# Optimization experiments

Measured on AMD Instinct MI355X. Metric: run time of the kernel, lower is better.

The kernel has to match this reference:

```python
import jax, jax.numpy as jnp
import numpy as np

D_MODEL = 1024
N_HEADS = 16
FEA = 512
BATCH = 16
D_FF = 2048
HALF = D_MODEL // 2  # d_model / 2**fd_num with fd_num=1
INV_SQRT2 = 1.0 / np.sqrt(2.0).astype(np.float32)


def conv1d_circ(x, w, b):
    # x: (B, C_in, L); w: (C_out, C_in, 3); circular padding of 1 each side
    xp = jnp.pad(x, ((0, 0), (0, 0), (1, 1)), mode='wrap')
    y = jax.lax.conv_general_dilated(xp, w, (1,), 'VALID',
                                     dimension_numbers=('NCH', 'OIH', 'NCH'))
    return y + b[None, :, None]


def layer_norm(x, g, b):
    m = jnp.mean(x, axis=-1, keepdims=True)
    v = jnp.mean((x - m) ** 2, axis=-1, keepdims=True)
    return (x - m) / jnp.sqrt(v + 1e-5) * g + b


def setup_inputs() -> dict:
    key = jax.random.key(0)
    ks = jax.random.split(key, 16)
    s = 0.02
    inp = {
        'x': jax.random.normal(ks[0], (BATCH, FEA, D_MODEL), dtype=jnp.float32),
        'Wq': jax.random.normal(ks[1], (D_MODEL, HALF, 3), dtype=jnp.float32) * s,
        'bq': jnp.zeros((D_MODEL,), jnp.float32),
        'Wk': jax.random.normal(ks[2], (D_MODEL, HALF, 3), dtype=jnp.float32) * s,
        'bk': jnp.zeros((D_MODEL,), jnp.float32),
        'Wv': jax.random.normal(ks[3], (D_MODEL, HALF, 3), dtype=jnp.float32) * s,
        'bv': jnp.zeros((D_MODEL,), jnp.float32),
        'uns_w': jax.random.normal(ks[4], (FEA, 2 * FEA, 3), dtype=jnp.float32) * s,
        'uns_b': jnp.zeros((FEA,), jnp.float32),
        'cv_w1': jax.random.normal(ks[5], (D_FF, D_MODEL, 3), dtype=jnp.float32) * s,
        'cv_b1': jnp.zeros((D_FF,), jnp.float32),
        'cv_w2': jax.random.normal(ks[6], (HALF, D_FF, 3), dtype=jnp.float32) * s,
        'cv_b2': jnp.zeros((HALF,), jnp.float32),
        'cv_g': jnp.ones((HALF,), jnp.float32),
        'cv_beta': jnp.zeros((HALF,), jnp.float32),
        'up_w1': jax.random.normal(ks[7], (D_FF, HALF, 3), dtype=jnp.float32) * s,
        'up_b1': jnp.zeros((D_FF,), jnp.float32),
        'up_w2': jax.random.normal(ks[8], (D_MODEL, D_FF, 3), dtype=jnp.float32) * s,
        'up_b2': jnp.zeros((D_MODEL,), jnp.float32),
        'up_g': jnp.ones((D_MODEL,), jnp.float32),
        'up_beta': jnp.zeros((D_MODEL,), jnp.float32),
    }
    return inp


def reference(x, Wq, bq, Wk, bk, Wv, bv, uns_w, uns_b,
              cv_w1, cv_b1, cv_w2, cv_b2, cv_g, cv_beta,
              up_w1, up_b1, up_w2, up_b2, up_g, up_beta):
    x_input = x
    # torch code detaches x before the wavelet transform -> no grad through this branch
    xd = jax.lax.stop_gradient(x)
    # Haar (db1) single-level DWT along last axis (even length -> exact pairwise)
    x1 = (xd[..., 0::2] + xd[..., 1::2]) * INV_SQRT2  # cA: (B, F, HALF)
    x2 = (xd[..., 0::2] - xd[..., 1::2]) * INV_SQRT2  # cD: (B, F, HALF)

    def proj(z, w, b):  # (B, F, HALF) -> (B, F, D_MODEL)
        return conv1d_circ(z.swapaxes(1, 2), w, b).swapaxes(1, 2)

    def heads(z):  # (B, F, D_MODEL) -> (B, H, F, dh)
        b_, f_, _ = z.shape
        return z.reshape(b_, f_, N_HEADS, -1).transpose(0, 2, 1, 3)

    qh, kh, vh = heads(proj(x1, Wq, bq)), heads(proj(x1, Wk, bk)), heads(proj(x1, Wv, bv))
    ql, kl, vl = heads(proj(x2, Wq, bq)), heads(proj(x2, Wk, bk)), heads(proj(x2, Wv, bv))

    scale = 1.0 / np.sqrt(N_HEADS).astype(np.float32)  # note: module scales by sqrt(n_heads)
    b_, f_ = x.shape[0], x.shape[1]

    hp = jax.nn.softmax(jnp.einsum('bhqd,bhkd->bhqk', qh, kl) * scale, axis=-1)
    h_ctx = jnp.einsum('bhqk,bhkd->bhqd', hp, vh).transpose(0, 2, 1, 3).reshape(b_, f_, -1)
    lp = jax.nn.softmax(jnp.einsum('bhqd,bhkd->bhqk', ql, kh) * scale, axis=-1)
    l_ctx = jnp.einsum('bhqk,bhkd->bhqd', lp, vl).transpose(0, 2, 1, 3).reshape(b_, f_, -1)

    ctx = jnp.concatenate([h_ctx, l_ctx], axis=1)          # (B, 2F, D_MODEL)
    ctx = conv1d_circ(ctx, uns_w, uns_b)                    # channels=2F -> F, length=D_MODEL

    # Convlayer: conv over fea axis, channels D_MODEL -> D_FF -> HALF, then LN
    h = conv1d_circ(ctx.swapaxes(1, 2), cv_w1, cv_b1)
    h = conv1d_circ(jax.nn.relu(h), cv_w2, cv_b2)
    ctx = layer_norm(h.swapaxes(1, 2), cv_g, cv_beta)       # (B, F, HALF)

    # upsizeConvlayer: HALF -> D_FF -> D_MODEL, then LN
    h = conv1d_circ(ctx.swapaxes(1, 2), up_w1, up_b1)
    h = conv1d_circ(jax.nn.relu(h), up_w2, up_b2)
    out = layer_norm(h.swapaxes(1, 2), up_g, up_beta)       # (B, F, D_MODEL)
    return out + x_input
```

## Files before the change

kernel.cpp:

```cpp
#include <hip/hip_runtime.h>
#include <hip/hip_bf16.h>

#define B_    16
#define FEA_  512
#define DM_   1024
#define HALF_ 512
#define DFF_  2048

typedef unsigned short u16;
typedef __attribute__((ext_vector_type(8))) short bf16x8;
typedef __attribute__((ext_vector_type(4))) float f32x4;

__device__ __forceinline__ float bf2f(u16 u) {
  union { unsigned int i; float f; } v; v.i = ((unsigned int)u) << 16; return v.f;
}
__device__ __forceinline__ u16 f2bf(float f) {
  union { float f; unsigned int i; } v; v.f = f;
  unsigned int x = v.i;
  return (u16)((x + 0x7fffu + ((x >> 16) & 1u)) >> 16);
}
__device__ __forceinline__ void gload16(const u16* g, u16* l) {
  __builtin_amdgcn_global_load_lds(
      (const __attribute__((address_space(1))) void*)g,
      (__attribute__((address_space(3))) void*)l, 16, 0, 0);
}

__global__ void dwt_kernel(const float* __restrict__ x, u16* __restrict__ x1,
                           u16* __restrict__ x2, int n) {
  int i = blockIdx.x * 256 + threadIdx.x;
  if (i >= n) return;
  float2 v = ((const float2*)x)[i];
  x1[i] = f2bf((v.x + v.y) * 0.70710678118f);
  x2[i] = f2bf((v.x - v.y) * 0.70710678118f);
}

__global__ void wtrans3_kernel(const float* __restrict__ w0, const float* __restrict__ w1,
                               const float* __restrict__ w2, u16* __restrict__ wt,
                               int Cout, int Cin) {
  int n = Cout * Cin * 3;
  int e = blockIdx.x * 256 + threadIdx.x;
  if (e >= 3 * n) return;
  int i = e / n, le = e - i * n;
  const float* w = (i == 0) ? w0 : ((i == 1) ? w1 : w2);
  int co = le / (Cin * 3);
  int r  = le - co * Cin * 3;
  int ci = r / 3;
  int t  = r - ci * 3;
  wt[(size_t)i * n + ((size_t)t * Cout + co) * Cin + ci] = f2bf(w[le]);
}

struct WTSeg { const float* src; u16* dst; int cout, cin, base; };
struct WT5 { WTSeg s[5]; int total; };
__global__ void wtrans5_kernel(WT5 p) {
  int e = blockIdx.x * 256 + threadIdx.x;
  if (e >= p.total) return;
#pragma unroll
  for (int i = 0; i < 5; ++i) {
    int Cin = p.s[i].cin, Cout = p.s[i].cout;
    int n = Cout * Cin * 3;
    int le = e - p.s[i].base;
    if (le >= 0 && le < n) {
      int co = le / (Cin * 3);
      int r  = le - co * Cin * 3;
      int ci = r / 3;
      int t  = r - ci * 3;
      p.s[i].dst[((size_t)t * Cout + co) * Cin + ci] = f2bf(p.s[i].src[le]);
    }
  }
}

#define ZS_GLOAD(c0_)                                                        \
  {                                                                          \
    _Pragma("unroll") for (int i_ = 0; i_ < 5; ++i_) {                       \
      int e_ = tid + i_ * 256;                                               \
      if (e_ < 130 * 8) {                                                    \
        int r_ = e_ >> 3, c_ = e_ & 7;                                       \
        int gl_ = l0 + r_ - 1;                                               \
        if (gl_ < 0) gl_ += L; else if (gl_ >= L) gl_ -= L;                  \
        gload16(Zb + (size_t)gl_ * Cin + (c0_) + ((c_ ^ (r_ & 7)) * 8),      \
                smem + ((size_t)(i_ * 256 + (tid & 192)) * 8));              \
      }                                                                      \
    }                                                                        \
  }
#define WS_ISSUE(t_, c0_, buf_)                                              \
  {                                                                          \
    const u16* Wg_ = Wt + ((size_t)(t_) * Cout + co0) * Cin + (c0_);         \
    int c_ = lane & 7;                                                       \
    _Pragma("unroll") for (int i_ = 0; i_ < 4; ++i_) {                       \
      int rw_ = (i_ * 4 + w) * 8 + (lane >> 3);                              \
      gload16(Wg_ + (size_t)rw_ * Cin + ((c_ ^ (rw_ & 7)) * 8),              \
              &Wb[(buf_)][(i_ * 4 + w) * 8][0]);                             \
    }                                                                        \
  }
#define COMPUTE(t_, buf_)                                                    \
  {                                                                          \
    _Pragma("unroll") for (int ks = 0; ks < 2; ++ks) {                       \
      int s = ks * 4 + g4;                                                   \
      bf16x8 af[4], bfr[4];                                                  \
      _Pragma("unroll") for (int mi = 0; mi < 4; ++mi) {                     \
        int ra = wr * 64 + mi * 16 + row16 + (t_);                           \
        af[mi] = *(const bf16x8*)&Zs[ra][(s ^ (ra & 7)) * 8];                \
      }                                                                      \
      _Pragma("unroll") for (int ni = 0; ni < 4; ++ni) {                     \
        int rb = wc * 64 + ni * 16 + row16;                                  \
        bfr[ni] = *(const bf16x8*)&Wb[(buf_)][rb][(s ^ (rb & 7)) * 8];       \
      }                                                                      \
      __builtin_amdgcn_s_setprio(1);                                         \
      _Pragma("unroll") for (int mi = 0; mi < 4; ++mi)                       \
        _Pragma("unroll") for (int ni = 0; ni < 4; ++ni)                     \
          acc[mi][ni] = __builtin_amdgcn_mfma_f32_16x16x32_bf16(             \
              af[mi], bfr[ni], acc[mi][ni], 0, 0, 0);                        \
      __builtin_amdgcn_s_setprio(0);                                         \
    }                                                                        \
  }
#define COMPUTE2_REG(buf_)                                                   \
  {                                                                          \
    _Pragma("unroll") for (int ks = 0; ks < 2; ++ks) {                       \
      int s = ks * 4 + g4;                                                   \
      bf16x8 bfr[4];                                                         \
      _Pragma("unroll") for (int ni = 0; ni < 4; ++ni) {                     \
        int rb = wc * 64 + ni * 16 + row16;                                  \
        bfr[ni] = *(const bf16x8*)&Wb[(buf_)][rb][(s ^ (rb & 7)) * 8];       \
      }                                                                      \
      __builtin_amdgcn_s_setprio(1);                                         \
      _Pragma("unroll") for (int mi = 0; mi < 4; ++mi)                       \
        _Pragma("unroll") for (int ni = 0; ni < 4; ++ni)                     \
          acc[mi][ni] = __builtin_amdgcn_mfma_f32_16x16x32_bf16(             \
              af2[ks * 4 + mi], bfr[ni], acc[mi][ni], 0, 0, 0);              \
      __builtin_amdgcn_s_setprio(0);                                         \
    }                                                                        \
  }
#define WAIT4 { asm volatile("s_waitcnt vmcnt(4)" ::: "memory");             \
                __builtin_amdgcn_s_barrier(); }

__global__ __launch_bounds__(256, 2) void conv_mfma_kernel(
    const u16* __restrict__ Z, const u16* __restrict__ Wt,
    const float* __restrict__ bias, u16* __restrict__ out,
    int L, int Cin, int Cout, int osl, int osc, int relu) {
  __shared__ __align__(16) u16 smem[130 * 64 + 3 * 128 * 64];
  u16 (*Zs)[64] = (u16(*)[64])smem;
  u16 (*Wb)[128][64] = (u16(*)[128][64])(smem + 130 * 64);
  int l0 = blockIdx.x * 128, co0 = blockIdx.y * 128, b = blockIdx.z;
  int tid = threadIdx.x;
  int lane = tid & 63, w = tid >> 6, wr = w >> 1, wc = w & 1;
  int row16 = lane & 15, g4 = lane >> 4;
  f32x4 acc[4][4];
#pragma unroll
  for (int i = 0; i < 4; ++i)
#pragma unroll
    for (int j = 0; j < 4; ++j) acc[i][j] = (f32x4){0.f, 0.f, 0.f, 0.f};
  const u16* Zb = Z + (size_t)b * L * Cin;

  int ncg = Cin >> 6;
  ZS_GLOAD(0);
  WS_ISSUE(0, 0, 0);
  WS_ISSUE(1, 0, 1);

  for (int cg = 0; cg < ncg; ++cg) {
    int c0 = cg << 6;
    bool lastg = (cg == ncg - 1);
    WAIT4;
    WS_ISSUE(2, c0, 2);
    COMPUTE(0, 0);
    WAIT4;
    if (!lastg) WS_ISSUE(0, c0 + 64, 0);
    COMPUTE(1, 1);
    if (!lastg) {
      WAIT4;
      bf16x8 af2[8];
#pragma unroll
      for (int ks = 0; ks < 2; ++ks) {
        int s = ks * 4 + g4;
#pragma unroll
        for (int mi = 0; mi < 4; ++mi) {
          int ra = wr * 64 + mi * 16 + row16 + 2;
          af2[ks * 4 + mi] = *(const bf16x8*)&Zs[ra][(s ^ (ra & 7)) * 8];
        }
      }
      __builtin_amdgcn_sched_barrier(0);
      asm volatile("s_waitcnt lgkmcnt(0)" ::: "memory");
      __builtin_amdgcn_s_barrier();
      ZS_GLOAD(c0 + 64);
      WS_ISSUE(1, c0 + 64, 1);
      COMPUTE2_REG(2);
    } else {
      asm volatile("s_waitcnt vmcnt(0)" ::: "memory");
      __builtin_amdgcn_s_barrier();
      COMPUTE(2, 2);
    }
  }

  __syncthreads();
  const int TP = 136;
  u16* tile = smem;
  size_t ob = (size_t)b * L * Cout;
  int S, rowbase, colbase;
  if (osc == 1) { S = osl; rowbase = l0; colbase = co0; }
  else          { S = osc; rowbase = co0; colbase = l0; }
#pragma unroll
  for (int ni = 0; ni < 4; ++ni) {
    int c_loc = wc * 64 + ni * 16 + row16;
    float bz = bias[co0 + c_loc];
#pragma unroll
    for (int mi = 0; mi < 4; ++mi) {
#pragma unroll
      for (int r = 0; r < 4; ++r) {
        int l_loc = wr * 64 + mi * 16 + g4 * 4 + r;
        float v = acc[mi][ni][r] + bz;
        if (relu) v = fmaxf(v, 0.f);
        int row = (osc == 1) ? l_loc : c_loc;
        int col = (osc == 1) ? c_loc : l_loc;
        tile[row * TP + col] = f2bf(v);
      }
    }
  }
  __syncthreads();
  for (int e = tid; e < 128 * 16; e += 256) {
    int row = e >> 4, c8 = (e & 15) * 8;
    *(uint4*)(out + ob + (size_t)(rowbase + row) * S + colbase + c8) =
        *(const uint4*)&tile[row * TP + c8];
  }
}

__global__ __launch_bounds__(256, 4) void attn_mfma_kernel(
    const u16* __restrict__ qh, const u16* __restrict__ kh, const u16* __restrict__ vhT,
    const u16* __restrict__ ql, const u16* __restrict__ kl, const u16* __restrict__ vlT,
    u16* __restrict__ ctx) {
  __shared__ u16 Qs[64][72], Ks[64][72], Vts[64][72];
  __shared__ u16 Ps[64][72];
  __shared__ float rsl[2][2][32];
  int qt = blockIdx.x, h = blockIdx.y, bz = blockIdx.z;
  int b = bz >> 1, br = bz & 1;
  const u16* Q  = br ? ql  : qh;
  const u16* K  = br ? kh  : kl;
  const u16* Vt = br ? vlT : vhT;
  int tid = threadIdx.x;
  int lane = tid & 63, w = tid >> 6, wr = w >> 1, wc = w & 1;
  int row16 = lane & 15, g4 = lane >> 4, k8 = g4 * 8;
  int q0 = qt * 64;
  size_t baseQK = (size_t)b * FEA_ * DM_ + h * 64;
  size_t baseV  = (size_t)b * DM_ * FEA_ + (size_t)(h * 64) * FEA_;
  for (int e = tid; e < 64 * 8; e += 256) {
    int r = e >> 3, c = e & 7;
    *(uint4*)&Qs[r][c * 8] = *(const uint4*)(Q + baseQK + (size_t)(q0 + r) * DM_ + c * 8);
  }
  f32x4 oacc[2][2];
  float rsum[2][4];
#pragma unroll
  for (int i = 0; i < 2; ++i) {
#pragma unroll
    for (int j = 0; j < 2; ++j) oacc[i][j] = (f32x4){0.f, 0.f, 0.f, 0.f};
#pragma unroll
    for (int r = 0; r < 4; ++r) rsum[i][r] = 0.f;
  }
  for (int kt = 0; kt < 8; ++kt) {
    __syncthreads();
    for (int e = tid; e < 64 * 8; e += 256) {
      int r = e >> 3, c = e & 7;
      *(uint4*)&Ks[r][c * 8]  = *(const uint4*)(K + baseQK + (size_t)(kt * 64 + r) * DM_ + c * 8);
      *(uint4*)&Vts[r][c * 8] = *(const uint4*)(Vt + baseV + (size_t)r * FEA_ + kt * 64 + c * 8);
    }
    __syncthreads();
    f32x4 sacc[2][2];
#pragma unroll
    for (int i = 0; i < 2; ++i)
#pragma unroll
      for (int j = 0; j < 2; ++j) sacc[i][j] = (f32x4){0.f, 0.f, 0.f, 0.f};
#pragma unroll
    for (int ks = 0; ks < 2; ++ks) {
      int k0 = ks * 32 + k8;
      bf16x8 a0 = *(const bf16x8*)&Qs[wr * 32 + row16][k0];
      bf16x8 a1 = *(const bf16x8*)&Qs[wr * 32 + 16 + row16][k0];
      bf16x8 b0 = *(const bf16x8*)&Ks[wc * 32 + row16][k0];
      bf16x8 b1 = *(const bf16x8*)&Ks[wc * 32 + 16 + row16][k0];
      sacc[0][0] = __builtin_amdgcn_mfma_f32_16x16x32_bf16(a0, b0, sacc[0][0], 0, 0, 0);
      sacc[0][1] = __builtin_amdgcn_mfma_f32_16x16x32_bf16(a0, b1, sacc[0][1], 0, 0, 0);
      sacc[1][0] = __builtin_amdgcn_mfma_f32_16x16x32_bf16(a1, b0, sacc[1][0], 0, 0, 0);
      sacc[1][1] = __builtin_amdgcn_mfma_f32_16x16x32_bf16(a1, b1, sacc[1][1], 0, 0, 0);
    }
#pragma unroll
    for (int mi = 0; mi < 2; ++mi)
#pragma unroll
      for (int ni = 0; ni < 2; ++ni)
#pragma unroll
        for (int r = 0; r < 4; ++r) {
          float p = __expf(sacc[mi][ni][r] * 0.25f);
          rsum[mi][r] += p;
          Ps[wr * 32 + mi * 16 + g4 * 4 + r][wc * 32 + ni * 16 + row16] = f2bf(p);
        }
    __syncthreads();
#pragma unroll
    for (int ks = 0; ks < 2; ++ks) {
      int k0 = ks * 32 + k8;
      bf16x8 a0 = *(const bf16x8*)&Ps[wr * 32 + row16][k0];
      bf16x8 a1 = *(const bf16x8*)&Ps[wr * 32 + 16 + row16][k0];
      bf16x8 b0 = *(const bf16x8*)&Vts[wc * 32 + row16][k0];
      bf16x8 b1 = *(const bf16x8*)&Vts[wc * 32 + 16 + row16][k0];
      oacc[0][0] = __builtin_amdgcn_mfma_f32_16x16x32_bf16(a0, b0, oacc[0][0], 0, 0, 0);
      oacc[0][1] = __builtin_amdgcn_mfma_f32_16x16x32_bf16(a0, b1, oacc[0][1], 0, 0, 0);
      oacc[1][0] = __builtin_amdgcn_mfma_f32_16x16x32_bf16(a1, b0, oacc[1][0], 0, 0, 0);
      oacc[1][1] = __builtin_amdgcn_mfma_f32_16x16x32_bf16(a1, b1, oacc[1][1], 0, 0, 0);
    }
  }
#pragma unroll
  for (int mi = 0; mi < 2; ++mi)
#pragma unroll
    for (int r = 0; r < 4; ++r) {
#pragma unroll
      for (int m = 1; m < 16; m <<= 1) rsum[mi][r] += __shfl_xor(rsum[mi][r], m);
    }
  if (row16 == 0) {
#pragma unroll
    for (int mi = 0; mi < 2; ++mi)
#pragma unroll
      for (int r = 0; r < 4; ++r) rsl[wr][wc][mi * 16 + g4 * 4 + r] = rsum[mi][r];
  }
  __syncthreads();
#pragma unroll
  for (int mi = 0; mi < 2; ++mi)
#pragma unroll
    for (int ni = 0; ni < 2; ++ni)
#pragma unroll
      for (int r = 0; r < 4; ++r) {
        int qq = mi * 16 + g4 * 4 + r;
        float denom = rsl[wr][0][qq] + rsl[wr][1][qq];
        float o = oacc[mi][ni][r] / denom;
        Ps[wc * 32 + ni * 16 + row16][wr * 32 + qq] = f2bf(o);
      }
  __syncthreads();
  for (int e = tid; e < 64 * 8; e += 256) {
    int r = e >> 3, c = e & 7;
    size_t dst = ((size_t)b * DM_ + h * 64 + r) * (2 * FEA_) + br * 512 + q0 + c * 8;
    *(uint4*)(ctx + dst) = *(const uint4*)&Ps[r][c * 8];
  }
}

template <int RESID>
__global__ void ln_kernel(const u16* __restrict__ in, const float* __restrict__ g,
                          const float* __restrict__ beta, const float* __restrict__ resid,
                          void* __restrict__ outp, int C) {
  int row = blockIdx.x;
  int tid = threadIdx.x;
  const u16* p = in + (size_t)row * C;
  float s = 0.f, ss = 0.f;
  for (int c = tid * 4; c < C; c += 1024) {
    ushort4 u = *(const ushort4*)(p + c);
    float v0 = bf2f(u.x), v1 = bf2f(u.y), v2 = bf2f(u.z), v3 = bf2f(u.w);
    s += v0 + v1 + v2 + v3;
    ss += v0 * v0 + v1 * v1 + v2 * v2 + v3 * v3;
  }
#pragma unroll
  for (int m = 1; m < 64; m <<= 1) { s += __shfl_xor(s, m); ss += __shfl_xor(ss, m); }
  __shared__ float red[2][4];
  int wid = tid >> 6, lane = tid & 63;
  if (lane == 0) { red[0][wid] = s; red[1][wid] = ss; }
  __syncthreads();
  s  = red[0][0] + red[0][1] + red[0][2] + red[0][3];
  ss = red[1][0] + red[1][1] + red[1][2] + red[1][3];
  float m  = s / C;
  float var = ss / C - m * m;
  float inv = rsqrtf(var + 1e-5f);
  for (int c = tid * 4; c < C; c += 1024) {
    ushort4 u = *(const ushort4*)(p + c);
    float4 gg = *(const float4*)(g + c);
    float4 bb = *(const float4*)(beta + c);
    float v0 = (bf2f(u.x) - m) * inv * gg.x + bb.x;
    float v1 = (bf2f(u.y) - m) * inv * gg.y + bb.y;
    float v2 = (bf2f(u.z) - m) * inv * gg.z + bb.z;
    float v3 = (bf2f(u.w) - m) * inv * gg.w + bb.w;
    if (RESID) {
      float4 rr = *(const float4*)(resid + (size_t)row * C + c);
      float4 o = {v0 + rr.x, v1 + rr.y, v2 + rr.z, v3 + rr.w};
      *(float4*)((float*)outp + (size_t)row * C + c) = o;
    } else {
      ushort4 o = {f2bf(v0), f2bf(v1), f2bf(v2), f2bf(v3)};
      *(ushort4*)((u16*)outp + (size_t)row * C + c) = o;
    }
  }
}

extern "C" void kernel_launch(void* const* d_in, const int* in_sizes, int n_in,
                              void* d_out, int out_size, void* d_ws, size_t ws_size,
                              hipStream_t stream) {
  (void)in_sizes; (void)n_in; (void)out_size; (void)ws_size;
  const float* x      = (const float*)d_in[0];
  const float* Wq     = (const float*)d_in[1];
  const float* bq     = (const float*)d_in[2];
  const float* Wk     = (const float*)d_in[3];
  const float* bk     = (const float*)d_in[4];
  const float* Wv     = (const float*)d_in[5];
  const float* bv     = (const float*)d_in[6];
  const float* uns_w  = (const float*)d_in[7];
  const float* uns_b  = (const float*)d_in[8];
  const float* cv_w1  = (const float*)d_in[9];
  const float* cv_b1  = (const float*)d_in[10];
  const float* cv_w2  = (const float*)d_in[11];
  const float* cv_b2  = (const float*)d_in[12];
  const float* cv_g   = (const float*)d_in[13];
  const float* cv_beta= (const float*)d_in[14];
  const float* up_w1  = (const float*)d_in[15];
  const float* up_b1  = (const float*)d_in[16];
  const float* up_w2  = (const float*)d_in[17];
  const float* up_b2  = (const float*)d_in[18];
  const float* up_g   = (const float*)d_in[19];
  const float* up_beta= (const float*)d_in[20];

  char* ws = (char*)d_ws;
  const size_t MB = 1ull << 20;
  u16* x1    = (u16*)(ws + 0);
  u16* x1x2  = x1;
  u16* qhb   = (u16*)(ws + 16 * MB);
  u16* khb   = (u16*)(ws + 48 * MB);
  u16* vhb   = (u16*)(ws + 80 * MB);
  u16* qlb   = (u16*)(ws + 32 * MB);
  u16* klb   = (u16*)(ws + 64 * MB);
  u16* vlb   = (u16*)(ws + 96 * MB);
  u16* wt_proj = (u16*)d_out;
  u16* ctx   = (u16*)d_out;
  u16* wt_uns  = (u16*)(ws + 0);
  u16* wt_cv1  = (u16*)(ws + 4 * MB);
  u16* wt_cv2  = (u16*)(ws + 17 * MB);
  u16* wt_up1  = (u16*)(ws + 24 * MB);
  u16* wt_up2  = (u16*)(ws + 31 * MB);
  u16* ctx2  = (u16*)(ws + 48 * MB);
  u16* h1    = (u16*)(ws + 64 * MB);
  u16* h2    = (u16*)(ws + 96 * MB);
  u16* ctx3  = (u16*)(ws + 104 * MB);
  u16* h3    = (u16*)(ws + 64 * MB);
  u16* h4    = (u16*)(ws + 48 * MB);

  dwt_kernel<<<(B_ * FEA_ * HALF_ + 255) / 256, 256, 0, stream>>>(x, x1, (u16*)(ws + 8 * MB),
                                                                  B_ * FEA_ * HALF_);

  const int NPROJ = DM_ * HALF_ * 3;
  wtrans3_kernel<<<(3 * NPROJ + 255) / 256, 256, 0, stream>>>(Wq, Wk, Wv, wt_proj, DM_, HALF_);

  auto conv = [&](const u16* Z, const u16* wt, const float* bias, u16* out, int L,
                  int Cin, int Cout, int osl, int osc, int relu, int nb) {
    conv_mfma_kernel<<<dim3(L / 128, Cout / 128, nb), 256, 0, stream>>>(
        Z, wt, bias, out, L, Cin, Cout, osl, osc, relu);
  };

  conv(x1x2, wt_proj,              bq, qhb, FEA_, HALF_, DM_, DM_, 1, 0, 32);
  conv(x1x2, wt_proj + NPROJ,      bk, khb, FEA_, HALF_, DM_, DM_, 1, 0, 32);
  conv(x1x2, wt_proj + 2 * NPROJ,  bv, vhb, FEA_, HALF_, DM_, 1, FEA_, 0, 32);

  attn_mfma_kernel<<<dim3(8, 16, 32), 256, 0, stream>>>(qhb, khb, vhb, qlb, klb, vlb, ctx);

  WT5 p;
  int base = 0;
  auto seg = [&](int i, const float* src, u16* dst, int cout, int cin) {
    p.s[i] = {src, dst, cout, cin, base};
    base += cout * cin * 3;
  };
  seg(0, uns_w, wt_uns, FEA_, 2 * FEA_);
  seg(1, cv_w1, wt_cv1, DFF_, DM_);
  seg(2, cv_w2, wt_cv2, HALF_, DFF_);
  seg(3, up_w1, wt_up1, DFF_, HALF_);
  seg(4, up_w2, wt_up2, DM_, DFF_);
  p.total = base;
  wtrans5_kernel<<<(p.total + 255) / 256, 256, 0, stream>>>(p);

  conv(ctx, wt_uns, uns_b, ctx2, DM_, 2 * FEA_, FEA_, 1, DM_, 0, B_);

  conv(ctx2, wt_cv1, cv_b1, h1, FEA_, DM_, DFF_, DFF_, 1, 1, B_);
  conv(h1, wt_cv2, cv_b2, h2, FEA_, DFF_, HALF_, HALF_, 1, 0, B_);
  ln_kernel<0><<<B_ * FEA_, 256, 0, stream>>>(h2, cv_g, cv_beta, nullptr, ctx3, HALF_);

  conv(ctx3, wt_up1, up_b1, h3, FEA_, HALF_, DFF_, DFF_, 1, 1, B_);
  conv(h3, wt_up2, up_b2, h4, FEA_, DFF_, DM_, DM_, 1, 0, B_);
  ln_kernel<1><<<B_ * FEA_, 256, 0, stream>>>(h4, up_g, up_beta, x, d_out, DM_);
}
```

Measured before the change: 663.6 us.

## Pipeline attention K/V loads with triple-buffered async LDS and 128-query tiles

```diff
diff --git a/kernel.cpp b/kernel.cpp
--- a/kernel.cpp
+++ b/kernel.cpp
@@ -222,116 +222,172 @@
   }
 }
 
-__global__ __launch_bounds__(256, 4) void attn_mfma_kernel(
+#define AQOFF 0
+#define AKOFF 8192
+#define AVOFF 20480
+#define APOFF 32768
+#define AT_Q_STAGE()                                                         \
+  { _Pragma("unroll") for (int i_ = 0; i_ < 4; ++i_) {                       \
+      int idx_ = tid + i_ * 256; int r_ = idx_ >> 3, c_ = idx_ & 7;          \
+      gload16(Qg + (size_t)(q0 + r_) * DM_ + ((c_ ^ (r_ & 7)) * 8),          \
+              asm_ + AQOFF + (i_ * 256 + (tid & 192)) * 8); } }
+#define AT_K_STAGE(kt_, buf_)                                                \
+  { _Pragma("unroll") for (int i_ = 0; i_ < 2; ++i_) {                       \
+      int idx_ = tid + i_ * 256; int r_ = idx_ >> 3, c_ = idx_ & 7;          \
+      gload16(Kg + (size_t)((kt_) * 64 + r_) * DM_ + ((c_ ^ (r_ & 7)) * 8),  \
+              asm_ + AKOFF + (buf_) * 4096 + (i_ * 256 + (tid & 192)) * 8); } }
+#define AT_V_STAGE(kt_, buf_)                                                \
+  { _Pragma("unroll") for (int i_ = 0; i_ < 2; ++i_) {                       \
+      int idx_ = tid + i_ * 256; int r_ = idx_ >> 3, c_ = idx_ & 7;          \
+      gload16(Vg + (size_t)r_ * FEA_ + (kt_) * 64 + ((c_ ^ (r_ & 7)) * 8),   \
+              asm_ + AVOFF + (buf_) * 4096 + (i_ * 256 + (tid & 192)) * 8); } }
+#define LGKM0_BAR { asm volatile("s_waitcnt lgkmcnt(0)" ::: "memory");       \
+                    __builtin_amdgcn_s_barrier(); }
+
+__global__ __launch_bounds__(256, 2) void attn_mfma_kernel(
     const u16* __restrict__ qh, const u16* __restrict__ kh, const u16* __restrict__ vhT,
     const u16* __restrict__ ql, const u16* __restrict__ kl, const u16* __restrict__ vlT,
     u16* __restrict__ ctx) {
-  __shared__ u16 Qs[64][72], Ks[64][72], Vts[64][72];
-  __shared__ u16 Ps[64][72];
-  __shared__ float rsl[2][2][32];
+  __shared__ __align__(16) u16 asm_[36864];
+  __shared__ float rsl[2][2][2][32];
   int qt = blockIdx.x, h = blockIdx.y, bz = blockIdx.z;
   int b = bz >> 1, br = bz & 1;
-  const u16* Q  = br ? ql  : qh;
-  const u16* K  = br ? kh  : kl;
-  const u16* Vt = br ? vlT : vhT;
+  const u16* Qg = (br ? ql  : qh) + (size_t)b * FEA_ * DM_ + h * 64;
+  const u16* Kg = (br ? kh  : kl) + (size_t)b * FEA_ * DM_ + h * 64;
+  const u16* Vg = (br ? vlT : vhT) + (size_t)b * DM_ * FEA_ + (size_t)(h * 64) * FEA_;
   int tid = threadIdx.x;
   int lane = tid & 63, w = tid >> 6, wr = w >> 1, wc = w & 1;
-  int row16 = lane & 15, g4 = lane >> 4, k8 = g4 * 8;
-  int q0 = qt * 64;
-  size_t baseQK = (size_t)b * FEA_ * DM_ + h * 64;
-  size_t baseV  = (size_t)b * DM_ * FEA_ + (size_t)(h * 64) * FEA_;
-  for (int e = tid; e < 64 * 8; e += 256) {
-    int r = e >> 3, c = e & 7;
-    *(uint4*)&Qs[r][c * 8] = *(const uint4*)(Q + baseQK + (size_t)(q0 + r) * DM_ + c * 8);
-  }
-  f32x4 oacc[2][2];
-  float rsum[2][4];
-#pragma unroll
-  for (int i = 0; i < 2; ++i) {
-#pragma unroll
-    for (int j = 0; j < 2; ++j) oacc[i][j] = (f32x4){0.f, 0.f, 0.f, 0.f};
-#pragma unroll
-    for (int r = 0; r < 4; ++r) rsum[i][r] = 0.f;
-  }
+  int row16 = lane & 15, g4 = lane >> 4;
+  int q0 = qt * 128;
+
+  f32x4 oacc[2][2][2];
+  float rsum[2][2][4];
+#pragma unroll
+  for (int qi = 0; qi < 2; ++qi)
+#pragma unroll
+    for (int i = 0; i < 2; ++i) {
+#pragma unroll
+      for (int j = 0; j < 2; ++j) oacc[qi][i][j] = (f32x4){0.f, 0.f, 0.f, 0.f};
+#pragma unroll
+      for (int r = 0; r < 4; ++r) rsum[qi][i][r] = 0.f;
+    }
+
+  AT_Q_STAGE();
+  AT_K_STAGE(0, 0); AT_V_STAGE(0, 0);
+  AT_K_STAGE(1, 1); AT_V_STAGE(1, 1);
+
   for (int kt = 0; kt < 8; ++kt) {
-    __syncthreads();
-    for (int e = tid; e < 64 * 8; e += 256) {
-      int r = e >> 3, c = e & 7;
-      *(uint4*)&Ks[r][c * 8]  = *(const uint4*)(K + baseQK + (size_t)(kt * 64 + r) * DM_ + c * 8);
-      *(uint4*)&Vts[r][c * 8] = *(const uint4*)(Vt + baseV + (size_t)r * FEA_ + kt * 64 + c * 8);
-    }
-    __syncthreads();
-    f32x4 sacc[2][2];
-#pragma unroll
-    for (int i = 0; i < 2; ++i)
-#pragma unroll
-      for (int j = 0; j < 2; ++j) sacc[i][j] = (f32x4){0.f, 0.f, 0.f, 0.f};
-#pragma unroll
-    for (int ks = 0; ks < 2; ++ks) {
-      int k0 = ks * 32 + k8;
-      bf16x8 a0 = *(const bf16x8*)&Qs[wr * 32 + row16][k0];
-      bf16x8 a1 = *(const bf16x8*)&Qs[wr * 32 + 16 + row16][k0];
-      bf16x8 b0 = *(const bf16x8*)&Ks[wc * 32 + row16][k0];
-      bf16x8 b1 = *(const bf16x8*)&Ks[wc * 32 + 16 + row16][k0];
-      sacc[0][0] = __builtin_amdgcn_mfma_f32_16x16x32_bf16(a0, b0, sacc[0][0], 0, 0, 0);
-      sacc[0][1] = __builtin_amdgcn_mfma_f32_16x16x32_bf16(a0, b1, sacc[0][1], 0, 0, 0);
-      sacc[1][0] = __builtin_amdgcn_mfma_f32_16x16x32_bf16(a1, b0, sacc[1][0], 0, 0, 0);
-      sacc[1][1] = __builtin_amdgcn_mfma_f32_16x16x32_bf16(a1, b1, sacc[1][1], 0, 0, 0);
-    }
+    int buf = kt % 3;
+    if (kt < 7) asm volatile("s_waitcnt vmcnt(4)" ::: "memory");
+    else        asm volatile("s_waitcnt vmcnt(0)" ::: "memory");
+    __builtin_amdgcn_s_barrier();
+    if (kt < 6) { AT_K_STAGE(kt + 2, (kt + 2) % 3); AT_V_STAGE(kt + 2, (kt + 2) % 3); }
+#pragma unroll
+    for (int qi = 0; qi < 2; ++qi) {
+      f32x4 sacc[2][2];
+#pragma unroll
+      for (int i = 0; i < 2; ++i)
+#pragma unroll
+        for (int j = 0; j < 2; ++j) sacc[i][j] = (f32x4){0.f, 0.f, 0.f, 0.f};
+#pragma unroll
+      for (int ks = 0; ks < 2; ++ks) {
+        int s = ks * 4 + g4;
+        bf16x8 a0, a1, b0, b1;
+        { int ra = qi * 64 + wr * 32 + row16;
+          a0 = *(const bf16x8*)&asm_[AQOFF + ra * 64 + ((s ^ (ra & 7)) * 8)]; }
+        { int ra = qi * 64 + wr * 32 + 16 + row16;
+          a1 = *(const bf16x8*)&asm_[AQOFF + ra * 64 + ((s ^ (ra & 7)) * 8)]; }
+        { int rb = wc * 32 + row16;
+          b0 = *(const bf16x8*)&asm_[AKOFF + buf * 4096 + rb * 64 + ((s ^ (rb & 7)) * 8)]; }
+        { int rb = wc * 32 + 16 + row16;
+          b1 = *(const bf16x8*)&asm_[AKOFF + buf * 4096 + rb * 64 + ((s ^ (rb & 7)) * 8)]; }
+        __builtin_amdgcn_s_setprio(1);
+        sacc[0][0] = __builtin_amdgcn_mfma_f32_16x16x32_bf16(a0, b0, sacc[0][0], 0, 0, 0);
+        sacc[0][1] = __builtin_amdgcn_mfma_f32_16x16x32_bf16(a0, b1, sacc[0][1], 0, 0, 0);
+        sacc[1][0] = __builtin_amdgcn_mfma_f32_16x16x32_bf16(a1, b0, sacc[1][0], 0, 0, 0);
+        sacc[1][1] = __builtin_amdgcn_mfma_f32_16x16x32_bf16(a1, b1, sacc[1][1], 0, 0, 0);
+        __builtin_amdgcn_s_setprio(0);
+      }
+      if (qi == 1) { LGKM0_BAR; }
+#pragma unroll
+      for (int mi = 0; mi < 2; ++mi)
+#pragma unroll
+        for (int ni = 0; ni < 2; ++ni)
+#pragma unroll
+          for (int r = 0; r < 4; ++r) {
+            float p = __expf(sacc[mi][ni][r] * 0.25f);
+            rsum[qi][mi][r] += p;
+            int pr = wr * 32 + mi * 16 + g4 * 4 + r;
+            int ck = wc * 32 + ni * 16 + row16;
+            asm_[APOFF + pr * 64 + (((ck >> 3) ^ (pr & 7)) * 8 + (ck & 7))] = f2bf(p);
+          }
+      LGKM0_BAR;
+#pragma unroll
+      for (int ks = 0; ks < 2; ++ks) {
+        int s = ks * 4 + g4;
+        bf16x8 a0, a1, b0, b1;
+        { int pa = wr * 32 + row16;
+          a0 = *(const bf16x8*)&asm_[APOFF + pa * 64 + ((s ^ (pa & 7)) * 8)]; }
+        { int pa = wr * 32 + 16 + row16;
+          a1 = *(const bf16x8*)&asm_[APOFF + pa * 64 + ((s ^ (pa & 7)) * 8)]; }
+        { int rv = wc * 32 + row16;
+          b0 = *(const bf16x8*)&asm_[AVOFF + buf * 4096 + rv * 64 + ((s ^ (rv & 7)) * 8)]; }
+        { int rv = wc * 32 + 16 + row16;
+          b1 = *(const bf16x8*)&asm_[AVOFF + buf * 4096 + rv * 64 + ((s ^ (rv & 7)) * 8)]; }
+        __builtin_amdgcn_s_setprio(1);
+        oacc[qi][0][0] = __builtin_amdgcn_mfma_f32_16x16x32_bf16(a0, b0, oacc[qi][0][0], 0, 0, 0);
+        oacc[qi][0][1] = __builtin_amdgcn_mfma_f32_16x16x32_bf16(a0, b1, oacc[qi][0][1], 0, 0, 0);
+        oacc[qi][1][0] = __builtin_amdgcn_mfma_f32_16x16x32_bf16(a1, b0, oacc[qi][1][0], 0, 0, 0);
+        oacc[qi][1][1] = __builtin_amdgcn_mfma_f32_16x16x32_bf16(a1, b1, oacc[qi][1][1], 0, 0, 0);
+        __builtin_amdgcn_s_setprio(0);
+      }
+    }
+  }
+
+#pragma unroll
+  for (int qi = 0; qi < 2; ++qi)
 #pragma unroll
     for (int mi = 0; mi < 2; ++mi)
 #pragma unroll
+      for (int r = 0; r < 4; ++r) {
+#pragma unroll
+        for (int m = 1; m < 16; m <<= 1)
+          rsum[qi][mi][r] += __shfl_xor(rsum[qi][mi][r], m);
+      }
+  if (row16 == 0) {
+#pragma unroll
+    for (int qi = 0; qi < 2; ++qi)
+#pragma unroll
+      for (int mi = 0; mi < 2; ++mi)
+#pragma unroll
+        for (int r = 0; r < 4; ++r)
+          rsl[qi][wr][wc][mi * 16 + g4 * 4 + r] = rsum[qi][mi][r];
+  }
+  __syncthreads();
+#pragma unroll
+  for (int qi = 0; qi < 2; ++qi) {
+#pragma unroll
+    for (int mi = 0; mi < 2; ++mi)
+#pragma unroll
       for (int ni = 0; ni < 2; ++ni)
 #pragma unroll
         for (int r = 0; r < 4; ++r) {
-          float p = __expf(sacc[mi][ni][r] * 0.25f);
-          rsum[mi][r] += p;
-          Ps[wr * 32 + mi * 16 + g4 * 4 + r][wc * 32 + ni * 16 + row16] = f2bf(p);
+          int qq = mi * 16 + g4 * 4 + r;
+          float denom = rsl[qi][wr][0][qq] + rsl[qi][wr][1][qq];
+          float o = oacc[qi][mi][ni][r] / denom;
+          int d = wc * 32 + ni * 16 + row16;
+          int qc = wr * 32 + qq;
+          asm_[APOFF + d * 64 + (((qc >> 3) ^ (d & 7)) * 8 + (qc & 7))] = f2bf(o);
         }
     __syncthreads();
 #pragma unroll
-    for (int ks = 0; ks < 2; ++ks) {
-      int k0 = ks * 32 + k8;
-      bf16x8 a0 = *(const bf16x8*)&Ps[wr * 32 + row16][k0];
-      bf16x8 a1 = *(const bf16x8*)&Ps[wr * 32 + 16 + row16][k0];
-      bf16x8 b0 = *(const bf16x8*)&Vts[wc * 32 + row16][k0];
-      bf16x8 b1 = *(const bf16x8*)&Vts[wc * 32 + 16 + row16][k0];
-      oacc[0][0] = __builtin_amdgcn_mfma_f32_16x16x32_bf16(a0, b0, oacc[0][0], 0, 0, 0);
-      oacc[0][1] = __builtin_amdgcn_mfma_f32_16x16x32_bf16(a0, b1, oacc[0][1], 0, 0, 0);
-      oacc[1][0] = __builtin_amdgcn_mfma_f32_16x16x32_bf16(a1, b0, oacc[1][0], 0, 0, 0);
-      oacc[1][1] = __builtin_amdgcn_mfma_f32_16x16x32_bf16(a1, b1, oacc[1][1], 0, 0, 0);
-    }
-  }
-#pragma unroll
-  for (int mi = 0; mi < 2; ++mi)
-#pragma unroll
-    for (int r = 0; r < 4; ++r) {
-#pragma unroll
-      for (int m = 1; m < 16; m <<= 1) rsum[mi][r] += __shfl_xor(rsum[mi][r], m);
-    }
-  if (row16 == 0) {
-#pragma unroll
-    for (int mi = 0; mi < 2; ++mi)
-#pragma unroll
-      for (int r = 0; r < 4; ++r) rsl[wr][wc][mi * 16 + g4 * 4 + r] = rsum[mi][r];
-  }
-  __syncthreads();
-#pragma unroll
-  for (int mi = 0; mi < 2; ++mi)
-#pragma unroll
-    for (int ni = 0; ni < 2; ++ni)
-#pragma unroll
-      for (int r = 0; r < 4; ++r) {
-        int qq = mi * 16 + g4 * 4 + r;
-        float denom = rsl[wr][0][qq] + rsl[wr][1][qq];
-        float o = oacc[mi][ni][r] / denom;
-        Ps[wc * 32 + ni * 16 + row16][wr * 32 + qq] = f2bf(o);
-      }
-  __syncthreads();
-  for (int e = tid; e < 64 * 8; e += 256) {
-    int r = e >> 3, c = e & 7;
-    size_t dst = ((size_t)b * DM_ + h * 64 + r) * (2 * FEA_) + br * 512 + q0 + c * 8;
-    *(uint4*)(ctx + dst) = *(const uint4*)&Ps[r][c * 8];
+    for (int i = 0; i < 2; ++i) {
+      int idx = tid + i * 256;
+      int r = idx >> 3, c = idx & 7;
+      size_t dst = ((size_t)b * DM_ + h * 64 + r) * (2 * FEA_) + br * 512 + q0 + qi * 64 + c * 8;
+      *(uint4*)(ctx + dst) = *(const uint4*)&asm_[APOFF + r * 64 + ((c ^ (r & 7)) * 8)];
+    }
+    if (qi == 0) __syncthreads();
   }
 }
 
@@ -445,7 +501,7 @@
   conv(x1x2, wt_proj + NPROJ,      bk, khb, FEA_, HALF_, DM_, DM_, 1, 0, 32);
   conv(x1x2, wt_proj + 2 * NPROJ,  bv, vhb, FEA_, HALF_, DM_, 1, FEA_, 0, 32);
 
-  attn_mfma_kernel<<<dim3(8, 16, 32), 256, 0, stream>>>(qhb, khb, vhb, qlb, klb, vlb, ctx);
+  attn_mfma_kernel<<<dim3(4, 16, 32), 256, 0, stream>>>(qhb, khb, vhb, qlb, klb, vlb, ctx);
 
   WT5 p;
   int base = 0;
```

Measured after the change: 671.4 us. Within noise of the previous version (+1.2%).
